# Kernel tuning notes

Hardware: AMD Instinct MI355X
Metric: run time of the kernel (lower is better)

Reference implementation:

```python
import jax, jax.numpy as jnp
import numpy as np

PROBE = 1.0
ALPHA = 0.5


def setup_inputs() -> dict:
    key = jax.random.key(0)
    ks = jax.random.split(key, 8)
    B, L, D = 4096, 128, 64  # batch, n_cats (fields), d_embed
    NG, NL = 2, 2
    cat_indices = jax.random.randint(ks[0], (B, L), 0, L, dtype=jnp.int64)
    emb_table = jax.random.normal(ks[1], (L, D), dtype=jnp.float32)
    acc_w = jax.random.normal(ks[2], (D, D), dtype=jnp.float32) * (1.0 / np.sqrt(D))
    acc_b = jnp.zeros((D,), dtype=jnp.float32)
    gw = jax.random.normal(ks[3], (NG, D, D), dtype=jnp.float32) * (1.0 / np.sqrt(D))
    gb = jnp.zeros((NG, D), dtype=jnp.float32)
    lw = jax.random.normal(ks[4], (NL, D, D), dtype=jnp.float32) * (1.0 / np.sqrt(D))
    lb = jnp.zeros((NL, D), dtype=jnp.float32)
    return {"cat_indices": cat_indices, "emb_table": emb_table, "acc_w": acc_w,
            "acc_b": acc_b, "gw": gw, "gb": gb, "lw": lw, "lb": lb}


def reference(cat_indices, emb_table, acc_w, acc_b, gw, gb, lw, lb):
    B, L = cat_indices.shape
    # shallow embedding lookup: [B, L, D]
    emb = emb_table[cat_indices]
    # uniform + probe*I adjacency, row-normalized by (L + probe); identical per sample
    adj = (jnp.ones((L, L), emb.dtype) + PROBE * jnp.eye(L, dtype=emb.dtype)) / (L + PROBE)
    # global branch: adj @ (emb @ W) + b
    support = jnp.einsum('bld,de->ble', emb, acc_w)
    g = jnp.einsum('lm,bme->ble', adj, support) + acc_b
    g = jax.nn.relu(g)
    n_global = gw.shape[0]
    for i in range(n_global):
        g = jnp.einsum('bld,ed->ble', g, gw[i]) + gb[i]
        if i + 1 < n_global:
            g = jax.nn.relu(g)
    # local FM branch: 0.5 * ((sum e)^2 - sum e^2)  -> [B, D]
    s = jnp.sum(emb, axis=1)
    loc = 0.5 * (s * s - jnp.sum(emb * emb, axis=1))
    n_local = lw.shape[0]
    for i in range(n_local):
        loc = loc @ lw[i].T + lb[i]
        if i + 1 < n_local:
            loc = jax.nn.relu(loc)
    # broadcast local [B, D] against global [B, L, D]
    return ALPHA * g + (1.0 - ALPHA) * loc[:, None, :]
```

## Files before the change

kernel.cpp:

```cpp
#include <hip/hip_runtime.h>
#include <hip/hip_bf16.h>


typedef __attribute__((ext_vector_type(8))) short bf16x8;
typedef __attribute__((ext_vector_type(4))) float f32x4;
typedef __attribute__((ext_vector_type(2))) unsigned int u32x2;

#define RECIP129 (1.0f/129.0f)

static __device__ __forceinline__ unsigned int cvt_pk_bf16(float lo, float hi){
  unsigned int r;
  asm("v_cvt_pk_bf16_f32 %0, %1, %2" : "=v"(r) : "v"(lo), "v"(hi));
  return r;
}

__global__ __launch_bounds__(64) void prep_kernel(const float* __restrict__ emb,
                                                  const float* __restrict__ acc_w,
                                                  const float* __restrict__ lw,
                                                  const float* __restrict__ gw,
                                                  unsigned int* __restrict__ tsupb,
                                                  uint4* __restrict__ fragtab){
  const int e = threadIdx.x, blk = blockIdx.x;
  const int r = e & 15, h = e >> 4;
  if (blk < 128){
    float acc = 0.f;
    #pragma unroll
    for (int d = 0; d < 64; ++d) acc += emb[blk*64 + d] * acc_w[d*64 + e];
    acc *= RECIP129;
    float alo = __shfl(acc, 2*(e & 31));
    float ahi = __shfl(acc, 2*(e & 31) + 1);
    if (e < 32) tsupb[blk*32 + e] = cvt_pk_bf16(alo, ahi);
  } else if (blk < 144){
    int f = blk - 128;
    int layer = f >> 3, nt = (f >> 1) & 3, kc = f & 1;
    float sc = layer ? 0.5f : 1.0f;
    const float* p0 = gw + layer*4096 + (nt*16 + r)*64 + kc*32 + h*8;
    float4 a = *reinterpret_cast<const float4*>(p0);
    float4 c = *reinterpret_cast<const float4*>(p0 + 4);
    uint4 v;
    v.x = cvt_pk_bf16(sc*a.x, sc*a.y); v.y = cvt_pk_bf16(sc*a.z, sc*a.w);
    v.z = cvt_pk_bf16(sc*c.x, sc*c.y); v.w = cvt_pk_bf16(sc*c.z, sc*c.w);
    fragtab[f*64 + e] = v;
  } else if (blk < 176){
    int g = blk - 144;
    int sq = g >= 16; if (sq) g -= 16;
    int nt = g >> 2, kc = g & 3;
    const float* base = emb + (kc*32 + h*8)*64 + nt*16 + r;
    unsigned int q[4];
    #pragma unroll
    for (int j2 = 0; j2 < 4; ++j2){
      float x = base[(2*j2)*64], y = base[(2*j2 + 1)*64];
      if (sq){ x *= x; y *= y; }
      q[j2] = cvt_pk_bf16(x, y);
    }
    uint4 v; v.x=q[0]; v.y=q[1]; v.z=q[2]; v.w=q[3];
    fragtab[(16 + sq*16 + g)*64 + e] = v;
  } else if (blk < 184){
    int g = blk - 176;
    int nt = g >> 1, kc = g & 1;
    const float* base = acc_w + (kc*32 + h*8)*64 + nt*16 + r;
    unsigned int q[4];
    #pragma unroll
    for (int j2 = 0; j2 < 4; ++j2)
      q[j2] = cvt_pk_bf16(base[(2*j2)*64]*RECIP129, base[(2*j2+1)*64]*RECIP129);
    uint4 v; v.x=q[0]; v.y=q[1]; v.z=q[2]; v.w=q[3];
    fragtab[(48 + g)*64 + e] = v;
  } else {
    int g = blk - 184;
    int layer = g >> 3, nt = (g >> 1) & 3, kc = g & 1;
    const float* p0 = lw + layer*4096 + (nt*16 + r)*64 + kc*32 + h*8;
    float4 a = *reinterpret_cast<const float4*>(p0);
    float4 c = *reinterpret_cast<const float4*>(p0 + 4);
    uint4 v;
    v.x = cvt_pk_bf16(a.x, a.y); v.y = cvt_pk_bf16(a.z, a.w);
    v.z = cvt_pk_bf16(c.x, c.y); v.w = cvt_pk_bf16(c.z, c.w);
    fragtab[(56 + g)*64 + e] = v;
  }
}

__global__ __launch_bounds__(256) void perb_kernel(const int*   __restrict__ cat,
                                                   const float* __restrict__ acc_b,
                                                   const float* __restrict__ lb,
                                                   const float* __restrict__ gbias,
                                                   const uint4* __restrict__ fragtab,
                                                   float* __restrict__ u_pg,
                                                   float* __restrict__ loc2g){
  __shared__ int hist[16*128];
  __shared__ __align__(16) unsigned int cbf[16*64];
  __shared__ __align__(16) unsigned short srows[16*64];
  __shared__ __align__(16) unsigned short lrows[16*64];
  const int tid = threadIdx.x, w = tid >> 6, lane = tid & 63;
  const int r = lane & 15, h = lane >> 4;
  const int bbase = blockIdx.x * 16;
  const int n = w*16 + h*4;
  const unsigned int swzr = (unsigned)(r & 7) << 4;

  #pragma unroll
  for (int i = 0; i < 8; ++i) hist[tid*8 + i] = 0;

  bf16x8 af_s[4], af_q[4], aw[2], l0f[2], l1f[2];
  #pragma unroll
  for (int kc = 0; kc < 4; ++kc){
    af_s[kc] = __builtin_bit_cast(bf16x8, fragtab[(16 + w*4 + kc)*64 + lane]);
    af_q[kc] = __builtin_bit_cast(bf16x8, fragtab[(32 + w*4 + kc)*64 + lane]);
  }
  #pragma unroll
  for (int kc = 0; kc < 2; ++kc){
    aw[kc]  = __builtin_bit_cast(bf16x8, fragtab[(48 + w*2 + kc)*64 + lane]);
    l0f[kc] = __builtin_bit_cast(bf16x8, fragtab[(56 + w*2 + kc)*64 + lane]);
    l1f[kc] = __builtin_bit_cast(bf16x8, fragtab[(64 + w*2 + kc)*64 + lane]);
  }
  float accb[4], lb0v[4], bias05[4];
  #pragma unroll
  for (int reg = 0; reg < 4; ++reg){
    accb[reg]   = acc_b[n + reg];
    lb0v[reg]   = lb[n + reg];
    bias05[reg] = 0.5f*(lb[64 + n + reg] + gbias[64 + n + reg]);
  }

  __syncthreads();
  {
    int b_l = tid >> 4, l0 = (tid & 15) * 8;
    const int* cp = cat + (bbase + b_l)*128 + l0;
    int4 i0 = *reinterpret_cast<const int4*>(cp);
    int4 i1 = *reinterpret_cast<const int4*>(cp + 4);
    atomicAdd(&hist[b_l*128 + i0.x], 1); atomicAdd(&hist[b_l*128 + i0.y], 1);
    atomicAdd(&hist[b_l*128 + i0.z], 1); atomicAdd(&hist[b_l*128 + i0.w], 1);
    atomicAdd(&hist[b_l*128 + i1.x], 1); atomicAdd(&hist[b_l*128 + i1.y], 1);
    atomicAdd(&hist[b_l*128 + i1.z], 1); atomicAdd(&hist[b_l*128 + i1.w], 1);
  }
  __syncthreads();
  {
    int b_l = tid >> 4, c0 = (tid & 15) * 8;
    float f[8];
    #pragma unroll
    for (int i = 0; i < 8; ++i) f[i] = (float)hist[b_l*128 + c0 + i];
    uint4 v;
    v.x = cvt_pk_bf16(f[0], f[1]); v.y = cvt_pk_bf16(f[2], f[3]);
    v.z = cvt_pk_bf16(f[4], f[5]); v.w = cvt_pk_bf16(f[6], f[7]);
    *reinterpret_cast<uint4*>((char*)cbf + b_l*256 + ((unsigned)(c0*2) ^ ((unsigned)(b_l & 7) << 4))) = v;
  }
  __syncthreads();

  const char* crow = (const char*)cbf + r*256;
  f32x4 acc_s = {0,0,0,0}, acc_q = {0,0,0,0};
  #pragma unroll
  for (int kc = 0; kc < 4; ++kc){
    bf16x8 cf = __builtin_bit_cast(bf16x8,
        *reinterpret_cast<const uint4*>(crow + ((unsigned)(kc*64 + h*16) ^ swzr)));
    acc_s = __builtin_amdgcn_mfma_f32_16x16x32_bf16(af_s[kc], cf, acc_s, 0, 0, 0);
    acc_q = __builtin_amdgcn_mfma_f32_16x16x32_bf16(af_q[kc], cf, acc_q, 0, 0, 0);
  }

  char* srow = (char*)srows + r*128;
  char* lrow = (char*)lrows + r*128;
  const unsigned int off = ((unsigned)(w*32 + h*8)) ^ swzr;
  {
    u32x2 ps, pl;
    ps[0] = cvt_pk_bf16(acc_s[0], acc_s[1]);
    ps[1] = cvt_pk_bf16(acc_s[2], acc_s[3]);
    float l0 = 0.5f*(acc_s[0]*acc_s[0] - acc_q[0]);
    float l1 = 0.5f*(acc_s[1]*acc_s[1] - acc_q[1]);
    float l2 = 0.5f*(acc_s[2]*acc_s[2] - acc_q[2]);
    float l3 = 0.5f*(acc_s[3]*acc_s[3] - acc_q[3]);
    pl[0] = cvt_pk_bf16(l0, l1); pl[1] = cvt_pk_bf16(l2, l3);
    *reinterpret_cast<u32x2*>(srow + off) = ps;
    *reinterpret_cast<u32x2*>(lrow + off) = pl;
  }
  __syncthreads();

  f32x4 acc_u; acc_u[0]=accb[0]; acc_u[1]=accb[1]; acc_u[2]=accb[2]; acc_u[3]=accb[3];
  f32x4 acc_h = {0,0,0,0};
  #pragma unroll
  for (int kc = 0; kc < 2; ++kc){
    unsigned o = ((unsigned)(kc*64 + h*16)) ^ swzr;
    bf16x8 sb = __builtin_bit_cast(bf16x8, *reinterpret_cast<const uint4*>((char*)srows + r*128 + o));
    bf16x8 lf = __builtin_bit_cast(bf16x8, *reinterpret_cast<const uint4*>((char*)lrows + r*128 + o));
    acc_u = __builtin_amdgcn_mfma_f32_16x16x32_bf16(aw[kc],  sb, acc_u, 0, 0, 0);
    acc_h = __builtin_amdgcn_mfma_f32_16x16x32_bf16(l0f[kc], lf, acc_h, 0, 0, 0);
  }
  {
    float4 st; st.x = acc_u[0]; st.y = acc_u[1]; st.z = acc_u[2]; st.w = acc_u[3];
    *reinterpret_cast<float4*>(u_pg + (size_t)(bbase + r)*64 + n) = st;
  }
  __syncthreads();
  {
    u32x2 ph;
    ph[0] = cvt_pk_bf16(fmaxf(acc_h[0] + lb0v[0], 0.f), fmaxf(acc_h[1] + lb0v[1], 0.f));
    ph[1] = cvt_pk_bf16(fmaxf(acc_h[2] + lb0v[2], 0.f), fmaxf(acc_h[3] + lb0v[3], 0.f));
    *reinterpret_cast<u32x2*>(lrow + off) = ph;
  }
  __syncthreads();

  f32x4 acc2 = {0,0,0,0};
  #pragma unroll
  for (int kc = 0; kc < 2; ++kc){
    unsigned o = ((unsigned)(kc*64 + h*16)) ^ swzr;
    bf16x8 hf = __builtin_bit_cast(bf16x8, *reinterpret_cast<const uint4*>((char*)lrows + r*128 + o));
    acc2 = __builtin_amdgcn_mfma_f32_16x16x32_bf16(l1f[kc], hf, acc2, 0, 0, 0);
  }
  {
    float4 st;
    st.x = 0.5f*acc2[0] + bias05[0]; st.y = 0.5f*acc2[1] + bias05[1];
    st.z = 0.5f*acc2[2] + bias05[2]; st.w = 0.5f*acc2[3] + bias05[3];
    *reinterpret_cast<float4*>(loc2g + (size_t)(bbase + r)*64 + n) = st;
  }
}

__global__ __launch_bounds__(256) void fused_kernel(
    const int*          __restrict__ cat,
    const unsigned int* __restrict__ tsupb,
    const float*        __restrict__ u_pg,
    const float*        __restrict__ loc2g,
    const uint4*        __restrict__ fragtab,
    const float*        __restrict__ gbias,
    float*              __restrict__ out)
{
  __shared__ __align__(16) unsigned short ts[128*72];
  __shared__ __align__(16) unsigned short gbuf[4][16*64];

  const int tid = threadIdx.x, wid = tid >> 6, lane = tid & 63;
  const int b = blockIdx.x*4 + wid;
  const int r = lane & 15, h = lane >> 4;

  {
    int k = tid >> 1, half = tid & 1;
    const uint4* src = reinterpret_cast<const uint4*>(tsupb) + k*8 + half*4;
    char* rowp = (char*)&ts[k*72];
    unsigned int swz = (unsigned)(k & 3) << 4;
    #pragma unroll
    for (int i = 0; i < 4; ++i)
      *reinterpret_cast<uint4*>(rowp + ((unsigned)(half*64 + i*16) ^ swz)) = src[i];
  }

  int k0 = cat[b*128 + lane];
  int k1 = cat[b*128 + 64 + lane];

  float uf[16];
  #pragma unroll
  for (int kc = 0; kc < 2; ++kc){
    const float* up = u_pg + (size_t)b*64 + kc*32 + h*8;
    float4 a = *reinterpret_cast<const float4*>(up);
    float4 c = *reinterpret_cast<const float4*>(up + 4);
    uf[kc*8+0]=a.x; uf[kc*8+1]=a.y; uf[kc*8+2]=a.z; uf[kc*8+3]=a.w;
    uf[kc*8+4]=c.x; uf[kc*8+5]=c.y; uf[kc*8+6]=c.z; uf[kc*8+7]=c.w;
  }
  f32x4 c2i[4], gb0f[4];
  #pragma unroll
  for (int mt = 0; mt < 4; ++mt){
    float4 lv = *reinterpret_cast<const float4*>(loc2g + (size_t)b*64 + mt*16 + h*4);
    f32x4 t; t[0]=lv.x; t[1]=lv.y; t[2]=lv.z; t[3]=lv.w;
    c2i[mt] = t;
    float4 gv = *reinterpret_cast<const float4*>(gbias + mt*16 + h*4);
    f32x4 g; g[0]=gv.x; g[1]=gv.y; g[2]=gv.z; g[3]=gv.w;
    gb0f[mt] = g;
  }
  bf16x8 w0[4][2], w1[4][2];
  #pragma unroll
  for (int nt = 0; nt < 4; ++nt)
    #pragma unroll
    for (int kc = 0; kc < 2; ++kc){
      w0[nt][kc] = __builtin_bit_cast(bf16x8, fragtab[(nt*2 + kc)*64 + lane]);
      w1[nt][kc] = __builtin_bit_cast(bf16x8, fragtab[(8 + nt*2 + kc)*64 + lane]);
    }

  __syncthreads();

  char* myrowW = (char*)&gbuf[wid][0] + r*128;
  const unsigned int rsw8 = (unsigned)(r & 7) << 4;

  for (int tl = 0; tl < 8; ++tl){
    const int rowbase = b*128 + tl*16;
    int kk = __shfl(tl < 4 ? k0 : k1, (tl & 3)*16 + r);

    const char* trow = (const char*)&ts[kk*72];
    const unsigned int ksw = (unsigned)(kk & 3) << 4;
    bf16x8 a0[2];
    #pragma unroll
    for (int kc = 0; kc < 2; ++kc){
      uint4 wv = *reinterpret_cast<const uint4*>(trow + ((unsigned)(kc*64 + h*16) ^ ksw));
      unsigned int ow[4];
      const unsigned int* wp = &wv.x;
      #pragma unroll
      for (int q = 0; q < 4; ++q){
        unsigned int wq = wp[q];
        float lo = fmaxf(__uint_as_float(wq << 16)         + uf[kc*8 + 2*q],     0.f);
        float hi = fmaxf(__uint_as_float(wq & 0xffff0000u) + uf[kc*8 + 2*q + 1], 0.f);
        ow[q] = cvt_pk_bf16(lo, hi);
      }
      uint4 packed; packed.x=ow[0]; packed.y=ow[1]; packed.z=ow[2]; packed.w=ow[3];
      a0[kc] = __builtin_bit_cast(bf16x8, packed);
    }

    f32x4 acc1[4];
    #pragma unroll
    for (int nt = 0; nt < 4; ++nt) acc1[nt] = gb0f[nt];
    #pragma unroll
    for (int kc = 0; kc < 2; ++kc)
      #pragma unroll
      for (int nt = 0; nt < 4; ++nt)
        acc1[nt] = __builtin_amdgcn_mfma_f32_16x16x32_bf16(w0[nt][kc], a0[kc], acc1[nt], 0, 0, 0);

    #pragma unroll
    for (int nt = 0; nt < 4; ++nt){
      u32x2 p;
      p[0] = cvt_pk_bf16(fmaxf(acc1[nt][0], 0.f), fmaxf(acc1[nt][1], 0.f));
      p[1] = cvt_pk_bf16(fmaxf(acc1[nt][2], 0.f), fmaxf(acc1[nt][3], 0.f));
      *reinterpret_cast<u32x2*>(myrowW + ((unsigned)(nt*32 + h*8) ^ rsw8)) = p;
    }

    bf16x8 a1[2];
    #pragma unroll
    for (int kc = 0; kc < 2; ++kc)
      a1[kc] = __builtin_bit_cast(bf16x8,
                 *reinterpret_cast<const uint4*>(myrowW + ((unsigned)(kc*64 + h*16) ^ rsw8)));

    f32x4 acc2[4];
    #pragma unroll
    for (int mt = 0; mt < 4; ++mt) acc2[mt] = c2i[mt];
    #pragma unroll
    for (int kc = 0; kc < 2; ++kc)
      #pragma unroll
      for (int mt = 0; mt < 4; ++mt)
        acc2[mt] = __builtin_amdgcn_mfma_f32_16x16x32_bf16(w1[mt][kc], a1[kc], acc2[mt], 0, 0, 0);

    float* orow = out + (size_t)(rowbase + r)*64 + h*4;
    #pragma unroll
    for (int mt = 0; mt < 4; ++mt){
      float4 st;
      st.x = acc2[mt][0]; st.y = acc2[mt][1];
      st.z = acc2[mt][2]; st.w = acc2[mt][3];
      *reinterpret_cast<float4*>(orow + mt*16) = st;
    }
  }
}

extern "C" void kernel_launch(void* const* d_in, const int* in_sizes, int n_in,
                              void* d_out, int out_size, void* d_ws, size_t ws_size,
                              hipStream_t stream) {
  const int*   cat   = (const int*)  d_in[0];
  const float* emb   = (const float*)d_in[1];
  const float* acc_w = (const float*)d_in[2];
  const float* acc_b = (const float*)d_in[3];
  const float* gw    = (const float*)d_in[4];
  const float* gb    = (const float*)d_in[5];
  const float* lw    = (const float*)d_in[6];
  const float* lb    = (const float*)d_in[7];
  float* out = (float*)d_out;

  const int B = in_sizes[0] / 128;

  float* ws           = (float*)d_ws;
  unsigned int* tsupb = (unsigned int*)ws;
  uint4* fragtab      = (uint4*)(ws + 4096);
  float* u_pg         = ws + 4096 + 18432;
  float* loc2g        = u_pg + (size_t)B*64;

  hipLaunchKernelGGL(prep_kernel, dim3(200), dim3(64), 0, stream,
                     emb, acc_w, lw, gw, tsupb, fragtab);
  hipLaunchKernelGGL(perb_kernel, dim3(B/16), dim3(256), 0, stream,
                     cat, acc_b, lb, gb, fragtab, u_pg, loc2g);
  hipLaunchKernelGGL(fused_kernel, dim3(B/4), dim3(256), 0, stream,
                     cat, tsupb, u_pg, loc2g, fragtab, gb, out);
}
```

Before: 37.12 us.

## Fuse per-batch prep and main kernels into one 512-thread mega kernel

Merges the per-sample kernel (histogram, FM local branch, u vector) and the main output kernel into a single kernel with 8 waves per 16-sample block. Intermediates u and loc2 now stay in shared memory instead of going through global memory, and one launch is removed. Waves 4-7 load the table into LDS while waves 0-3 build the histogram. In exchange the grid drops from B/4 to B/16 blocks and each wave handles two samples serially. LDS use per block also rises, which may lower occupancy.

```diff
diff --git a/kernel.cpp b/kernel.cpp
--- a/kernel.cpp
+++ b/kernel.cpp
@@ -78,48 +78,74 @@
   }
 }
 
-__global__ __launch_bounds__(256) void perb_kernel(const int*   __restrict__ cat,
-                                                   const float* __restrict__ acc_b,
-                                                   const float* __restrict__ lb,
-                                                   const float* __restrict__ gbias,
-                                                   const uint4* __restrict__ fragtab,
-                                                   float* __restrict__ u_pg,
-                                                   float* __restrict__ loc2g){
+__global__ __launch_bounds__(512) void mega_kernel(
+    const int*          __restrict__ cat,
+    const unsigned int* __restrict__ tsupb,
+    const float*        __restrict__ acc_b,
+    const float*        __restrict__ lb,
+    const float*        __restrict__ gbias,
+    const uint4*        __restrict__ fragtab,
+    float*              __restrict__ out)
+{
   __shared__ int hist[16*128];
-  __shared__ __align__(16) unsigned int cbf[16*64];
+  __shared__ __align__(16) unsigned int  cbf[16*64];
   __shared__ __align__(16) unsigned short srows[16*64];
   __shared__ __align__(16) unsigned short lrows[16*64];
+  __shared__ float u_s[16][68];
+  __shared__ float l2_s[16][68];
+  __shared__ __align__(16) unsigned short ts[128*72];
+  __shared__ __align__(16) unsigned short gbuf[8][16*64];
+
   const int tid = threadIdx.x, w = tid >> 6, lane = tid & 63;
   const int r = lane & 15, h = lane >> 4;
   const int bbase = blockIdx.x * 16;
-  const int n = w*16 + h*4;
   const unsigned int swzr = (unsigned)(r & 7) << 4;
 
+  bf16x8 w0[4][2], w1[4][2];
   #pragma unroll
-  for (int i = 0; i < 8; ++i) hist[tid*8 + i] = 0;
+  for (int nt = 0; nt < 4; ++nt)
+    #pragma unroll
+    for (int kc = 0; kc < 2; ++kc){
+      w0[nt][kc] = __builtin_bit_cast(bf16x8, fragtab[(nt*2 + kc)*64 + lane]);
+      w1[nt][kc] = __builtin_bit_cast(bf16x8, fragtab[(8 + nt*2 + kc)*64 + lane]);
+    }
+  f32x4 gb0f[4];
+  #pragma unroll
+  for (int mt = 0; mt < 4; ++mt){
+    float4 gv = *reinterpret_cast<const float4*>(gbias + mt*16 + h*4);
+    f32x4 g; g[0]=gv.x; g[1]=gv.y; g[2]=gv.z; g[3]=gv.w;
+    gb0f[mt] = g;
+  }
 
   bf16x8 af_s[4], af_q[4], aw[2], l0f[2], l1f[2];
+  float accb[4], lb0v[4], bias05[4];
+  f32x4 acc_h = {0,0,0,0};
+  if (w < 4){
+    #pragma unroll
+    for (int kc = 0; kc < 4; ++kc){
+      af_s[kc] = __builtin_bit_cast(bf16x8, fragtab[(16 + w*4 + kc)*64 + lane]);
+      af_q[kc] = __builtin_bit_cast(bf16x8, fragtab[(32 + w*4 + kc)*64 + lane]);
+    }
+    #pragma unroll
+    for (int kc = 0; kc < 2; ++kc){
+      aw[kc]  = __builtin_bit_cast(bf16x8, fragtab[(48 + w*2 + kc)*64 + lane]);
+      l0f[kc] = __builtin_bit_cast(bf16x8, fragtab[(56 + w*2 + kc)*64 + lane]);
+      l1f[kc] = __builtin_bit_cast(bf16x8, fragtab[(64 + w*2 + kc)*64 + lane]);
+    }
+    const int n = w*16 + h*4;
+    #pragma unroll
+    for (int reg = 0; reg < 4; ++reg){
+      accb[reg]   = acc_b[n + reg];
+      lb0v[reg]   = lb[n + reg];
+      bias05[reg] = 0.5f*(lb[64 + n + reg] + gbias[64 + n + reg]);
+    }
+  }
+
   #pragma unroll
-  for (int kc = 0; kc < 4; ++kc){
-    af_s[kc] = __builtin_bit_cast(bf16x8, fragtab[(16 + w*4 + kc)*64 + lane]);
-    af_q[kc] = __builtin_bit_cast(bf16x8, fragtab[(32 + w*4 + kc)*64 + lane]);
-  }
-  #pragma unroll
-  for (int kc = 0; kc < 2; ++kc){
-    aw[kc]  = __builtin_bit_cast(bf16x8, fragtab[(48 + w*2 + kc)*64 + lane]);
-    l0f[kc] = __builtin_bit_cast(bf16x8, fragtab[(56 + w*2 + kc)*64 + lane]);
-    l1f[kc] = __builtin_bit_cast(bf16x8, fragtab[(64 + w*2 + kc)*64 + lane]);
-  }
-  float accb[4], lb0v[4], bias05[4];
-  #pragma unroll
-  for (int reg = 0; reg < 4; ++reg){
-    accb[reg]   = acc_b[n + reg];
-    lb0v[reg]   = lb[n + reg];
-    bias05[reg] = 0.5f*(lb[64 + n + reg] + gbias[64 + n + reg]);
-  }
-
-  __syncthreads();
-  {
+  for (int i = 0; i < 4; ++i) hist[tid*4 + i] = 0;
+  __syncthreads();
+
+  if (w < 4){
     int b_l = tid >> 4, l0 = (tid & 15) * 8;
     const int* cp = cat + (bbase + b_l)*128 + l0;
     int4 i0 = *reinterpret_cast<const int4*>(cp);
@@ -128,9 +154,19 @@
     atomicAdd(&hist[b_l*128 + i0.z], 1); atomicAdd(&hist[b_l*128 + i0.w], 1);
     atomicAdd(&hist[b_l*128 + i1.x], 1); atomicAdd(&hist[b_l*128 + i1.y], 1);
     atomicAdd(&hist[b_l*128 + i1.z], 1); atomicAdd(&hist[b_l*128 + i1.w], 1);
-  }
-  __syncthreads();
-  {
+  } else {
+    int t2 = tid - 256;
+    int k = t2 >> 1, half = t2 & 1;
+    const uint4* src = reinterpret_cast<const uint4*>(tsupb) + k*8 + half*4;
+    char* rowp = (char*)&ts[k*72];
+    unsigned int swz = (unsigned)(k & 3) << 4;
+    #pragma unroll
+    for (int i = 0; i < 4; ++i)
+      *reinterpret_cast<uint4*>(rowp + ((unsigned)(half*64 + i*16) ^ swz)) = src[i];
+  }
+  __syncthreads();
+
+  if (w < 4){
     int b_l = tid >> 4, c0 = (tid & 15) * 8;
     float f[8];
     #pragma unroll
@@ -142,49 +178,49 @@
   }
   __syncthreads();
 
-  const char* crow = (const char*)cbf + r*256;
-  f32x4 acc_s = {0,0,0,0}, acc_q = {0,0,0,0};
-  #pragma unroll
-  for (int kc = 0; kc < 4; ++kc){
-    bf16x8 cf = __builtin_bit_cast(bf16x8,
-        *reinterpret_cast<const uint4*>(crow + ((unsigned)(kc*64 + h*16) ^ swzr)));
-    acc_s = __builtin_amdgcn_mfma_f32_16x16x32_bf16(af_s[kc], cf, acc_s, 0, 0, 0);
-    acc_q = __builtin_amdgcn_mfma_f32_16x16x32_bf16(af_q[kc], cf, acc_q, 0, 0, 0);
-  }
-
-  char* srow = (char*)srows + r*128;
-  char* lrow = (char*)lrows + r*128;
-  const unsigned int off = ((unsigned)(w*32 + h*8)) ^ swzr;
-  {
+  if (w < 4){
+    const char* crow = (const char*)cbf + r*256;
+    f32x4 acc_s = {0,0,0,0}, acc_q = {0,0,0,0};
+    #pragma unroll
+    for (int kc = 0; kc < 4; ++kc){
+      bf16x8 cf = __builtin_bit_cast(bf16x8,
+          *reinterpret_cast<const uint4*>(crow + ((unsigned)(kc*64 + h*16) ^ swzr)));
+      acc_s = __builtin_amdgcn_mfma_f32_16x16x32_bf16(af_s[kc], cf, acc_s, 0, 0, 0);
+      acc_q = __builtin_amdgcn_mfma_f32_16x16x32_bf16(af_q[kc], cf, acc_q, 0, 0, 0);
+    }
+    char* srow = (char*)srows + r*128;
+    char* lrow = (char*)lrows + r*128;
+    const unsigned int off = ((unsigned)(w*32 + h*8)) ^ swzr;
     u32x2 ps, pl;
     ps[0] = cvt_pk_bf16(acc_s[0], acc_s[1]);
     ps[1] = cvt_pk_bf16(acc_s[2], acc_s[3]);
     float l0 = 0.5f*(acc_s[0]*acc_s[0] - acc_q[0]);
     float l1 = 0.5f*(acc_s[1]*acc_s[1] - acc_q[1]);
-    float l2 = 0.5f*(acc_s[2]*acc_s[2] - acc_q[2]);
+    float l2v = 0.5f*(acc_s[2]*acc_s[2] - acc_q[2]);
     float l3 = 0.5f*(acc_s[3]*acc_s[3] - acc_q[3]);
-    pl[0] = cvt_pk_bf16(l0, l1); pl[1] = cvt_pk_bf16(l2, l3);
+    pl[0] = cvt_pk_bf16(l0, l1); pl[1] = cvt_pk_bf16(l2v, l3);
     *reinterpret_cast<u32x2*>(srow + off) = ps;
     *reinterpret_cast<u32x2*>(lrow + off) = pl;
   }
   __syncthreads();
 
-  f32x4 acc_u; acc_u[0]=accb[0]; acc_u[1]=accb[1]; acc_u[2]=accb[2]; acc_u[3]=accb[3];
-  f32x4 acc_h = {0,0,0,0};
-  #pragma unroll
-  for (int kc = 0; kc < 2; ++kc){
-    unsigned o = ((unsigned)(kc*64 + h*16)) ^ swzr;
-    bf16x8 sb = __builtin_bit_cast(bf16x8, *reinterpret_cast<const uint4*>((char*)srows + r*128 + o));
-    bf16x8 lf = __builtin_bit_cast(bf16x8, *reinterpret_cast<const uint4*>((char*)lrows + r*128 + o));
-    acc_u = __builtin_amdgcn_mfma_f32_16x16x32_bf16(aw[kc],  sb, acc_u, 0, 0, 0);
-    acc_h = __builtin_amdgcn_mfma_f32_16x16x32_bf16(l0f[kc], lf, acc_h, 0, 0, 0);
-  }
-  {
-    float4 st; st.x = acc_u[0]; st.y = acc_u[1]; st.z = acc_u[2]; st.w = acc_u[3];
-    *reinterpret_cast<float4*>(u_pg + (size_t)(bbase + r)*64 + n) = st;
-  }
-  __syncthreads();
-  {
+  if (w < 4){
+    f32x4 acc_u; acc_u[0]=accb[0]; acc_u[1]=accb[1]; acc_u[2]=accb[2]; acc_u[3]=accb[3];
+    #pragma unroll
+    for (int kc = 0; kc < 2; ++kc){
+      unsigned o = ((unsigned)(kc*64 + h*16)) ^ swzr;
+      bf16x8 sb = __builtin_bit_cast(bf16x8, *reinterpret_cast<const uint4*>((char*)srows + r*128 + o));
+      bf16x8 lf = __builtin_bit_cast(bf16x8, *reinterpret_cast<const uint4*>((char*)lrows + r*128 + o));
+      acc_u = __builtin_amdgcn_mfma_f32_16x16x32_bf16(aw[kc],  sb, acc_u, 0, 0, 0);
+      acc_h = __builtin_amdgcn_mfma_f32_16x16x32_bf16(l0f[kc], lf, acc_h, 0, 0, 0);
+    }
+    f32x4 st; st[0]=acc_u[0]; st[1]=acc_u[1]; st[2]=acc_u[2]; st[3]=acc_u[3];
+    *reinterpret_cast<f32x4*>(&u_s[r][w*16 + h*4]) = st;
+  }
+  __syncthreads();
+  if (w < 4){
+    char* lrow = (char*)lrows + r*128;
+    const unsigned int off = ((unsigned)(w*32 + h*8)) ^ swzr;
     u32x2 ph;
     ph[0] = cvt_pk_bf16(fmaxf(acc_h[0] + lb0v[0], 0.f), fmaxf(acc_h[1] + lb0v[1], 0.f));
     ph[1] = cvt_pk_bf16(fmaxf(acc_h[2] + lb0v[2], 0.f), fmaxf(acc_h[3] + lb0v[3], 0.f));
@@ -192,145 +228,109 @@
   }
   __syncthreads();
 
-  f32x4 acc2 = {0,0,0,0};
-  #pragma unroll
-  for (int kc = 0; kc < 2; ++kc){
-    unsigned o = ((unsigned)(kc*64 + h*16)) ^ swzr;
-    bf16x8 hf = __builtin_bit_cast(bf16x8, *reinterpret_cast<const uint4*>((char*)lrows + r*128 + o));
-    acc2 = __builtin_amdgcn_mfma_f32_16x16x32_bf16(l1f[kc], hf, acc2, 0, 0, 0);
-  }
-  {
-    float4 st;
-    st.x = 0.5f*acc2[0] + bias05[0]; st.y = 0.5f*acc2[1] + bias05[1];
-    st.z = 0.5f*acc2[2] + bias05[2]; st.w = 0.5f*acc2[3] + bias05[3];
-    *reinterpret_cast<float4*>(loc2g + (size_t)(bbase + r)*64 + n) = st;
-  }
-}
-
-__global__ __launch_bounds__(256) void fused_kernel(
-    const int*          __restrict__ cat,
-    const unsigned int* __restrict__ tsupb,
-    const float*        __restrict__ u_pg,
-    const float*        __restrict__ loc2g,
-    const uint4*        __restrict__ fragtab,
-    const float*        __restrict__ gbias,
-    float*              __restrict__ out)
-{
-  __shared__ __align__(16) unsigned short ts[128*72];
-  __shared__ __align__(16) unsigned short gbuf[4][16*64];
-
-  const int tid = threadIdx.x, wid = tid >> 6, lane = tid & 63;
-  const int b = blockIdx.x*4 + wid;
-  const int r = lane & 15, h = lane >> 4;
-
-  {
-    int k = tid >> 1, half = tid & 1;
-    const uint4* src = reinterpret_cast<const uint4*>(tsupb) + k*8 + half*4;
-    char* rowp = (char*)&ts[k*72];
-    unsigned int swz = (unsigned)(k & 3) << 4;
-    #pragma unroll
-    for (int i = 0; i < 4; ++i)
-      *reinterpret_cast<uint4*>(rowp + ((unsigned)(half*64 + i*16) ^ swz)) = src[i];
-  }
-
-  int k0 = cat[b*128 + lane];
-  int k1 = cat[b*128 + 64 + lane];
-
-  float uf[16];
-  #pragma unroll
-  for (int kc = 0; kc < 2; ++kc){
-    const float* up = u_pg + (size_t)b*64 + kc*32 + h*8;
-    float4 a = *reinterpret_cast<const float4*>(up);
-    float4 c = *reinterpret_cast<const float4*>(up + 4);
-    uf[kc*8+0]=a.x; uf[kc*8+1]=a.y; uf[kc*8+2]=a.z; uf[kc*8+3]=a.w;
-    uf[kc*8+4]=c.x; uf[kc*8+5]=c.y; uf[kc*8+6]=c.z; uf[kc*8+7]=c.w;
-  }
-  f32x4 c2i[4], gb0f[4];
-  #pragma unroll
-  for (int mt = 0; mt < 4; ++mt){
-    float4 lv = *reinterpret_cast<const float4*>(loc2g + (size_t)b*64 + mt*16 + h*4);
-    f32x4 t; t[0]=lv.x; t[1]=lv.y; t[2]=lv.z; t[3]=lv.w;
-    c2i[mt] = t;
-    float4 gv = *reinterpret_cast<const float4*>(gbias + mt*16 + h*4);
-    f32x4 g; g[0]=gv.x; g[1]=gv.y; g[2]=gv.z; g[3]=gv.w;
-    gb0f[mt] = g;
-  }
-  bf16x8 w0[4][2], w1[4][2];
-  #pragma unroll
-  for (int nt = 0; nt < 4; ++nt)
+  if (w < 4){
+    f32x4 acc2 = {0,0,0,0};
     #pragma unroll
     for (int kc = 0; kc < 2; ++kc){
-      w0[nt][kc] = __builtin_bit_cast(bf16x8, fragtab[(nt*2 + kc)*64 + lane]);
-      w1[nt][kc] = __builtin_bit_cast(bf16x8, fragtab[(8 + nt*2 + kc)*64 + lane]);
-    }
-
-  __syncthreads();
-
-  char* myrowW = (char*)&gbuf[wid][0] + r*128;
+      unsigned o = ((unsigned)(kc*64 + h*16)) ^ swzr;
+      bf16x8 hf = __builtin_bit_cast(bf16x8, *reinterpret_cast<const uint4*>((char*)lrows + r*128 + o));
+      acc2 = __builtin_amdgcn_mfma_f32_16x16x32_bf16(l1f[kc], hf, acc2, 0, 0, 0);
+    }
+    f32x4 st;
+    st[0] = 0.5f*acc2[0] + bias05[0]; st[1] = 0.5f*acc2[1] + bias05[1];
+    st[2] = 0.5f*acc2[2] + bias05[2]; st[3] = 0.5f*acc2[3] + bias05[3];
+    *reinterpret_cast<f32x4*>(&l2_s[r][w*16 + h*4]) = st;
+  }
+  __syncthreads();
+
+  char* myrowW = (char*)&gbuf[w][0] + r*128;
   const unsigned int rsw8 = (unsigned)(r & 7) << 4;
 
-  for (int tl = 0; tl < 8; ++tl){
-    const int rowbase = b*128 + tl*16;
-    int kk = __shfl(tl < 4 ? k0 : k1, (tl & 3)*16 + r);
-
-    const char* trow = (const char*)&ts[kk*72];
-    const unsigned int ksw = (unsigned)(kk & 3) << 4;
-    bf16x8 a0[2];
-    #pragma unroll
-    for (int kc = 0; kc < 2; ++kc){
-      uint4 wv = *reinterpret_cast<const uint4*>(trow + ((unsigned)(kc*64 + h*16) ^ ksw));
-      unsigned int ow[4];
-      const unsigned int* wp = &wv.x;
-      #pragma unroll
-      for (int q = 0; q < 4; ++q){
-        unsigned int wq = wp[q];
-        float lo = fmaxf(__uint_as_float(wq << 16)         + uf[kc*8 + 2*q],     0.f);
-        float hi = fmaxf(__uint_as_float(wq & 0xffff0000u) + uf[kc*8 + 2*q + 1], 0.f);
-        ow[q] = cvt_pk_bf16(lo, hi);
+  for (int bi = 0; bi < 2; ++bi){
+    const int b_l = w*2 + bi;
+    const int b = bbase + b_l;
+    int ki0 = cat[b*128 + lane];
+    int ki1 = cat[b*128 + 64 + lane];
+
+    float uf[16];
+    #pragma unroll
+    for (int kc = 0; kc < 2; ++kc)
+      #pragma unroll
+      for (int j = 0; j < 8; ++j)
+        uf[kc*8 + j] = u_s[b_l][kc*32 + h*8 + j];
+
+    f32x4 c2i[4];
+    #pragma unroll
+    for (int mt = 0; mt < 4; ++mt){
+      f32x4 t;
+      t[0] = l2_s[b_l][mt*16 + h*4 + 0]; t[1] = l2_s[b_l][mt*16 + h*4 + 1];
+      t[2] = l2_s[b_l][mt*16 + h*4 + 2]; t[3] = l2_s[b_l][mt*16 + h*4 + 3];
+      c2i[mt] = t;
+    }
+
+    for (int tl = 0; tl < 8; ++tl){
+      const int rowbase = b*128 + tl*16;
+      int kk = __shfl(tl < 4 ? ki0 : ki1, (tl & 3)*16 + r);
+
+      const char* trow = (const char*)&ts[kk*72];
+      const unsigned int ksw = (unsigned)(kk & 3) << 4;
+      bf16x8 a0[2];
+      #pragma unroll
+      for (int kc = 0; kc < 2; ++kc){
+        uint4 wv = *reinterpret_cast<const uint4*>(trow + ((unsigned)(kc*64 + h*16) ^ ksw));
+        unsigned int ow[4];
+        const unsigned int* wp = &wv.x;
+        #pragma unroll
+        for (int q = 0; q < 4; ++q){
+          unsigned int wq = wp[q];
+          float lo = fmaxf(__uint_as_float(wq << 16)         + uf[kc*8 + 2*q],     0.f);
+          float hi = fmaxf(__uint_as_float(wq & 0xffff0000u) + uf[kc*8 + 2*q + 1], 0.f);
+          ow[q] = cvt_pk_bf16(lo, hi);
+        }
+        uint4 packed; packed.x=ow[0]; packed.y=ow[1]; packed.z=ow[2]; packed.w=ow[3];
+        a0[kc] = __builtin_bit_cast(bf16x8, packed);
       }
-      uint4 packed; packed.x=ow[0]; packed.y=ow[1]; packed.z=ow[2]; packed.w=ow[3];
-      a0[kc] = __builtin_bit_cast(bf16x8, packed);
-    }
-
-    f32x4 acc1[4];
-    #pragma unroll
-    for (int nt = 0; nt < 4; ++nt) acc1[nt] = gb0f[nt];
-    #pragma unroll
-    for (int kc = 0; kc < 2; ++kc)
-      #pragma unroll
-      for (int nt = 0; nt < 4; ++nt)
-        acc1[nt] = __builtin_amdgcn_mfma_f32_16x16x32_bf16(w0[nt][kc], a0[kc], acc1[nt], 0, 0, 0);
-
-    #pragma unroll
-    for (int nt = 0; nt < 4; ++nt){
-      u32x2 p;
-      p[0] = cvt_pk_bf16(fmaxf(acc1[nt][0], 0.f), fmaxf(acc1[nt][1], 0.f));
-      p[1] = cvt_pk_bf16(fmaxf(acc1[nt][2], 0.f), fmaxf(acc1[nt][3], 0.f));
-      *reinterpret_cast<u32x2*>(myrowW + ((unsigned)(nt*32 + h*8) ^ rsw8)) = p;
-    }
-
-    bf16x8 a1[2];
-    #pragma unroll
-    for (int kc = 0; kc < 2; ++kc)
-      a1[kc] = __builtin_bit_cast(bf16x8,
-                 *reinterpret_cast<const uint4*>(myrowW + ((unsigned)(kc*64 + h*16) ^ rsw8)));
-
-    f32x4 acc2[4];
-    #pragma unroll
-    for (int mt = 0; mt < 4; ++mt) acc2[mt] = c2i[mt];
-    #pragma unroll
-    for (int kc = 0; kc < 2; ++kc)
-      #pragma unroll
-      for (int mt = 0; mt < 4; ++mt)
-        acc2[mt] = __builtin_amdgcn_mfma_f32_16x16x32_bf16(w1[mt][kc], a1[kc], acc2[mt], 0, 0, 0);
-
-    float* orow = out + (size_t)(rowbase + r)*64 + h*4;
-    #pragma unroll
-    for (int mt = 0; mt < 4; ++mt){
-      float4 st;
-      st.x = acc2[mt][0]; st.y = acc2[mt][1];
-      st.z = acc2[mt][2]; st.w = acc2[mt][3];
-      *reinterpret_cast<float4*>(orow + mt*16) = st;
+
+      f32x4 acc1[4];
+      #pragma unroll
+      for (int nt = 0; nt < 4; ++nt) acc1[nt] = gb0f[nt];
+      #pragma unroll
+      for (int kc = 0; kc < 2; ++kc)
+        #pragma unroll
+        for (int nt = 0; nt < 4; ++nt)
+          acc1[nt] = __builtin_amdgcn_mfma_f32_16x16x32_bf16(w0[nt][kc], a0[kc], acc1[nt], 0, 0, 0);
+
+      #pragma unroll
+      for (int nt = 0; nt < 4; ++nt){
+        u32x2 p;
+        p[0] = cvt_pk_bf16(fmaxf(acc1[nt][0], 0.f), fmaxf(acc1[nt][1], 0.f));
+        p[1] = cvt_pk_bf16(fmaxf(acc1[nt][2], 0.f), fmaxf(acc1[nt][3], 0.f));
+        *reinterpret_cast<u32x2*>(myrowW + ((unsigned)(nt*32 + h*8) ^ rsw8)) = p;
+      }
+
+      bf16x8 a1[2];
+      #pragma unroll
+      for (int kc = 0; kc < 2; ++kc)
+        a1[kc] = __builtin_bit_cast(bf16x8,
+                   *reinterpret_cast<const uint4*>(myrowW + ((unsigned)(kc*64 + h*16) ^ rsw8)));
+
+      f32x4 acc2[4];
+      #pragma unroll
+      for (int mt = 0; mt < 4; ++mt) acc2[mt] = c2i[mt];
+      #pragma unroll
+      for (int kc = 0; kc < 2; ++kc)
+        #pragma unroll
+        for (int mt = 0; mt < 4; ++mt)
+          acc2[mt] = __builtin_amdgcn_mfma_f32_16x16x32_bf16(w1[mt][kc], a1[kc], acc2[mt], 0, 0, 0);
+
+      float* orow = out + (size_t)(rowbase + r)*64 + h*4;
+      #pragma unroll
+      for (int mt = 0; mt < 4; ++mt){
+        float4 st;
+        st.x = acc2[mt][0]; st.y = acc2[mt][1];
+        st.z = acc2[mt][2]; st.w = acc2[mt][3];
+        *reinterpret_cast<float4*>(orow + mt*16) = st;
+      }
     }
   }
 }
@@ -353,13 +353,9 @@
   float* ws           = (float*)d_ws;
   unsigned int* tsupb = (unsigned int*)ws;
   uint4* fragtab      = (uint4*)(ws + 4096);
-  float* u_pg         = ws + 4096 + 18432;
-  float* loc2g        = u_pg + (size_t)B*64;
 
   hipLaunchKernelGGL(prep_kernel, dim3(200), dim3(64), 0, stream,
                      emb, acc_w, lw, gw, tsupb, fragtab);
-  hipLaunchKernelGGL(perb_kernel, dim3(B/16), dim3(256), 0, stream,
-                     cat, acc_b, lb, gb, fragtab, u_pg, loc2g);
-  hipLaunchKernelGGL(fused_kernel, dim3(B/4), dim3(256), 0, stream,
-                     cat, tsupb, u_pg, loc2g, fragtab, gb, out);
+  hipLaunchKernelGGL(mega_kernel, dim3(B/16), dim3(512), 0, stream,
+                     cat, tsupb, acc_b, lb, gb, fragtab, out);
 }
```

Measured after the change: 37.00 us. No clear change (-0.3%).

## Merge prep kernel into per-batch kernel and build fragments from raw weights

Applied to the files above, without the earlier changes.

Removes the separate prep launch. The per-batch kernel blocks now build their own bf16 MFMA fragments for emb, emb squared, acc_w and lw directly from fp32 global memory, instead of reading precomputed fragment tables. Nine extra blocks in the same grid compute tsupb and the gw fragments that the later fused kernel needs. This saves one launch and one dependency, but every block redundantly reloads and converts weights with strided loads. The grid is hardcoded to 265, which assumes B=4096.

```diff
diff --git a/kernel.cpp b/kernel.cpp
--- a/kernel.cpp
+++ b/kernel.cpp
@@ -13,85 +13,68 @@
   asm("v_cvt_pk_bf16_f32 %0, %1, %2" : "=v"(r) : "v"(lo), "v"(hi));
   return r;
 }
-
-__global__ __launch_bounds__(64) void prep_kernel(const float* __restrict__ emb,
-                                                  const float* __restrict__ acc_w,
-                                                  const float* __restrict__ lw,
-                                                  const float* __restrict__ gw,
-                                                  unsigned int* __restrict__ tsupb,
-                                                  uint4* __restrict__ fragtab){
-  const int e = threadIdx.x, blk = blockIdx.x;
-  const int r = e & 15, h = e >> 4;
-  if (blk < 128){
-    float acc = 0.f;
-    #pragma unroll
-    for (int d = 0; d < 64; ++d) acc += emb[blk*64 + d] * acc_w[d*64 + e];
-    acc *= RECIP129;
-    float alo = __shfl(acc, 2*(e & 31));
-    float ahi = __shfl(acc, 2*(e & 31) + 1);
-    if (e < 32) tsupb[blk*32 + e] = cvt_pk_bf16(alo, ahi);
-  } else if (blk < 144){
-    int f = blk - 128;
-    int layer = f >> 3, nt = (f >> 1) & 3, kc = f & 1;
-    float sc = layer ? 0.5f : 1.0f;
-    const float* p0 = gw + layer*4096 + (nt*16 + r)*64 + kc*32 + h*8;
-    float4 a = *reinterpret_cast<const float4*>(p0);
-    float4 c = *reinterpret_cast<const float4*>(p0 + 4);
-    uint4 v;
-    v.x = cvt_pk_bf16(sc*a.x, sc*a.y); v.y = cvt_pk_bf16(sc*a.z, sc*a.w);
-    v.z = cvt_pk_bf16(sc*c.x, sc*c.y); v.w = cvt_pk_bf16(sc*c.z, sc*c.w);
-    fragtab[f*64 + e] = v;
-  } else if (blk < 176){
-    int g = blk - 144;
-    int sq = g >= 16; if (sq) g -= 16;
-    int nt = g >> 2, kc = g & 3;
-    const float* base = emb + (kc*32 + h*8)*64 + nt*16 + r;
-    unsigned int q[4];
-    #pragma unroll
-    for (int j2 = 0; j2 < 4; ++j2){
-      float x = base[(2*j2)*64], y = base[(2*j2 + 1)*64];
-      if (sq){ x *= x; y *= y; }
-      q[j2] = cvt_pk_bf16(x, y);
-    }
-    uint4 v; v.x=q[0]; v.y=q[1]; v.z=q[2]; v.w=q[3];
-    fragtab[(16 + sq*16 + g)*64 + e] = v;
-  } else if (blk < 184){
-    int g = blk - 176;
-    int nt = g >> 1, kc = g & 1;
-    const float* base = acc_w + (kc*32 + h*8)*64 + nt*16 + r;
-    unsigned int q[4];
-    #pragma unroll
-    for (int j2 = 0; j2 < 4; ++j2)
-      q[j2] = cvt_pk_bf16(base[(2*j2)*64]*RECIP129, base[(2*j2+1)*64]*RECIP129);
-    uint4 v; v.x=q[0]; v.y=q[1]; v.z=q[2]; v.w=q[3];
-    fragtab[(48 + g)*64 + e] = v;
-  } else {
-    int g = blk - 184;
-    int layer = g >> 3, nt = (g >> 1) & 3, kc = g & 1;
-    const float* p0 = lw + layer*4096 + (nt*16 + r)*64 + kc*32 + h*8;
-    float4 a = *reinterpret_cast<const float4*>(p0);
-    float4 c = *reinterpret_cast<const float4*>(p0 + 4);
-    uint4 v;
-    v.x = cvt_pk_bf16(a.x, a.y); v.y = cvt_pk_bf16(a.z, a.w);
-    v.z = cvt_pk_bf16(c.x, c.y); v.w = cvt_pk_bf16(c.z, c.w);
-    fragtab[(56 + g)*64 + e] = v;
-  }
-}
-
-__global__ __launch_bounds__(256) void perb_kernel(const int*   __restrict__ cat,
-                                                   const float* __restrict__ acc_b,
-                                                   const float* __restrict__ lb,
-                                                   const float* __restrict__ gbias,
-                                                   const uint4* __restrict__ fragtab,
-                                                   float* __restrict__ u_pg,
-                                                   float* __restrict__ loc2g){
+static __device__ __forceinline__ bf16x8 pack8(const float* v){
+  uint4 p;
+  p.x = cvt_pk_bf16(v[0], v[1]); p.y = cvt_pk_bf16(v[2], v[3]);
+  p.z = cvt_pk_bf16(v[4], v[5]); p.w = cvt_pk_bf16(v[6], v[7]);
+  return __builtin_bit_cast(bf16x8, p);
+}
+
+__global__ __launch_bounds__(256) void combined_kernel(
+    const int*   __restrict__ cat,
+    const float* __restrict__ emb,
+    const float* __restrict__ acc_w,
+    const float* __restrict__ acc_b,
+    const float* __restrict__ lw,
+    const float* __restrict__ lb,
+    const float* __restrict__ gw,
+    const float* __restrict__ gbias,
+    unsigned int* __restrict__ tsupb,
+    uint4* __restrict__ fragtab,
+    float* __restrict__ u_pg,
+    float* __restrict__ loc2g)
+{
+  const int tid = threadIdx.x;
+  const int blk = blockIdx.x;
+
+  if (blk >= 256){
+    if (blk < 264){
+      int local = blk - 256;
+      int k = local*16 + (tid >> 4), e0 = (tid & 15)*4;
+      float a0=0.f, a1=0.f, a2=0.f, a3=0.f;
+      for (int d = 0; d < 64; ++d){
+        float ev = emb[k*64 + d];
+        float4 wv = *reinterpret_cast<const float4*>(acc_w + d*64 + e0);
+        a0 += ev*wv.x; a1 += ev*wv.y; a2 += ev*wv.z; a3 += ev*wv.w;
+      }
+      tsupb[k*32 + (e0 >> 1)]     = cvt_pk_bf16(a0*RECIP129, a1*RECIP129);
+      tsupb[k*32 + (e0 >> 1) + 1] = cvt_pk_bf16(a2*RECIP129, a3*RECIP129);
+    } else {
+      int lane = tid & 63, r = lane & 15, h = lane >> 4;
+      #pragma unroll
+      for (int i = 0; i < 4; ++i){
+        int f = (tid >> 6) + i*4;
+        int layer = f >> 3, nt = (f >> 1) & 3, kc = f & 1;
+        float sc = layer ? 0.5f : 1.0f;
+        const float* p0 = gw + layer*4096 + (nt*16 + r)*64 + kc*32 + h*8;
+        float4 a = *reinterpret_cast<const float4*>(p0);
+        float4 c = *reinterpret_cast<const float4*>(p0 + 4);
+        uint4 v;
+        v.x = cvt_pk_bf16(sc*a.x, sc*a.y); v.y = cvt_pk_bf16(sc*a.z, sc*a.w);
+        v.z = cvt_pk_bf16(sc*c.x, sc*c.y); v.w = cvt_pk_bf16(sc*c.z, sc*c.w);
+        fragtab[f*64 + lane] = v;
+      }
+    }
+    return;
+  }
+
   __shared__ int hist[16*128];
   __shared__ __align__(16) unsigned int cbf[16*64];
   __shared__ __align__(16) unsigned short srows[16*64];
   __shared__ __align__(16) unsigned short lrows[16*64];
-  const int tid = threadIdx.x, w = tid >> 6, lane = tid & 63;
+  const int w = tid >> 6, lane = tid & 63;
   const int r = lane & 15, h = lane >> 4;
-  const int bbase = blockIdx.x * 16;
+  const int bbase = blk * 16;
   const int n = w*16 + h*4;
   const unsigned int swzr = (unsigned)(r & 7) << 4;
 
@@ -99,16 +82,34 @@
   for (int i = 0; i < 8; ++i) hist[tid*8 + i] = 0;
 
   bf16x8 af_s[4], af_q[4], aw[2], l0f[2], l1f[2];
-  #pragma unroll
-  for (int kc = 0; kc < 4; ++kc){
-    af_s[kc] = __builtin_bit_cast(bf16x8, fragtab[(16 + w*4 + kc)*64 + lane]);
-    af_q[kc] = __builtin_bit_cast(bf16x8, fragtab[(32 + w*4 + kc)*64 + lane]);
-  }
-  #pragma unroll
-  for (int kc = 0; kc < 2; ++kc){
-    aw[kc]  = __builtin_bit_cast(bf16x8, fragtab[(48 + w*2 + kc)*64 + lane]);
-    l0f[kc] = __builtin_bit_cast(bf16x8, fragtab[(56 + w*2 + kc)*64 + lane]);
-    l1f[kc] = __builtin_bit_cast(bf16x8, fragtab[(64 + w*2 + kc)*64 + lane]);
+  {
+    float vs[8], vq[8];
+    #pragma unroll
+    for (int kc = 0; kc < 4; ++kc){
+      #pragma unroll
+      for (int j = 0; j < 8; ++j){
+        float x = emb[(kc*32 + h*8 + j)*64 + w*16 + r];
+        vs[j] = x; vq[j] = x*x;
+      }
+      af_s[kc] = pack8(vs);
+      af_q[kc] = pack8(vq);
+    }
+    #pragma unroll
+    for (int kc = 0; kc < 2; ++kc){
+      #pragma unroll
+      for (int j = 0; j < 8; ++j)
+        vs[j] = acc_w[(kc*32 + h*8 + j)*64 + w*16 + r] * RECIP129;
+      aw[kc] = pack8(vs);
+      const float* p0 = lw + (w*16 + r)*64 + kc*32 + h*8;
+      float4 a = *reinterpret_cast<const float4*>(p0);
+      float4 c = *reinterpret_cast<const float4*>(p0 + 4);
+      float t0[8] = {a.x,a.y,a.z,a.w,c.x,c.y,c.z,c.w};
+      l0f[kc] = pack8(t0);
+      a = *reinterpret_cast<const float4*>(p0 + 4096);
+      c = *reinterpret_cast<const float4*>(p0 + 4100);
+      float t1[8] = {a.x,a.y,a.z,a.w,c.x,c.y,c.z,c.w};
+      l1f[kc] = pack8(t1);
+    }
   }
   float accb[4], lb0v[4], bias05[4];
   #pragma unroll
@@ -161,9 +162,9 @@
     ps[1] = cvt_pk_bf16(acc_s[2], acc_s[3]);
     float l0 = 0.5f*(acc_s[0]*acc_s[0] - acc_q[0]);
     float l1 = 0.5f*(acc_s[1]*acc_s[1] - acc_q[1]);
-    float l2 = 0.5f*(acc_s[2]*acc_s[2] - acc_q[2]);
+    float l2v = 0.5f*(acc_s[2]*acc_s[2] - acc_q[2]);
     float l3 = 0.5f*(acc_s[3]*acc_s[3] - acc_q[3]);
-    pl[0] = cvt_pk_bf16(l0, l1); pl[1] = cvt_pk_bf16(l2, l3);
+    pl[0] = cvt_pk_bf16(l0, l1); pl[1] = cvt_pk_bf16(l2v, l3);
     *reinterpret_cast<u32x2*>(srow + off) = ps;
     *reinterpret_cast<u32x2*>(lrow + off) = pl;
   }
@@ -353,13 +354,12 @@
   float* ws           = (float*)d_ws;
   unsigned int* tsupb = (unsigned int*)ws;
   uint4* fragtab      = (uint4*)(ws + 4096);
-  float* u_pg         = ws + 4096 + 18432;
+  float* u_pg         = ws + 8192;
   float* loc2g        = u_pg + (size_t)B*64;
 
-  hipLaunchKernelGGL(prep_kernel, dim3(200), dim3(64), 0, stream,
-                     emb, acc_w, lw, gw, tsupb, fragtab);
-  hipLaunchKernelGGL(perb_kernel, dim3(B/16), dim3(256), 0, stream,
-                     cat, acc_b, lb, gb, fragtab, u_pg, loc2g);
+  hipLaunchKernelGGL(combined_kernel, dim3(265), dim3(256), 0, stream,
+                     cat, emb, acc_w, acc_b, lw, lb, gw, gb,
+                     tsupb, fragtab, u_pg, loc2g);
   hipLaunchKernelGGL(fused_kernel, dim3(B/4), dim3(256), 0, stream,
                      cat, tsupb, u_pg, loc2g, fragtab, gb, out);
 }
```

New measurement: 35.90 us. -3.3%, faster.
